# Performance work log

Measured on AMD Instinct MI355X. Metric: run time of the kernel, lower is better.

## Reference

```python
import jax, jax.numpy as jnp
import numpy as np

N = 100000
SEQ = 12
DIMS = [32, 64, 64, 32]


def _glorot(key, shape):
    fan_in, fan_out = shape[0], shape[1]
    lim = jnp.sqrt(6.0 / (fan_in + fan_out))
    return jax.random.uniform(key, shape, jnp.float32, -lim, lim)


def setup_inputs() -> dict:
    key = jax.random.key(0)
    ks = jax.random.split(key, 8)
    x = jax.random.normal(ks[0], (N, DIMS[0], 1), dtype=jnp.float32)
    spiral_indices = jax.random.randint(ks[1], (N, SEQ), 0, N)
    # SpiralConv i: Linear(SEQ * DIMS[i], DIMS[i+1])
    W0 = _glorot(ks[2], (SEQ * DIMS[0], DIMS[1]))
    b0 = jnp.zeros((DIMS[1],), jnp.float32)
    W1 = _glorot(ks[3], (SEQ * DIMS[1], DIMS[2]))
    b1 = jnp.zeros((DIMS[2],), jnp.float32)
    W2 = _glorot(ks[4], (SEQ * DIMS[2], DIMS[3]))
    b2 = jnp.zeros((DIMS[3],), jnp.float32)
    return {"x": x, "spiral_indices": spiral_indices,
            "W0": W0, "b0": b0, "W1": W1, "b1": b1, "W2": W2, "b2": b2}


def _spiral_conv(h, idx, W, b):
    # h: [N, C]; idx: [N, SEQ] -> gathered [N, SEQ, C] -> flat [N, SEQ*C]
    n = h.shape[0]
    g = jnp.take(h, idx, axis=0).reshape(n, -1)
    return g @ W + b


def reference(x, spiral_indices, W0, b0, W1, b1, W2, b2):
    h = x[..., 0]  # squeeze(-1): [N, C_in]
    h = jax.nn.elu(_spiral_conv(h, spiral_indices, W0, b0))
    h = jax.nn.elu(_spiral_conv(h, spiral_indices, W1, b1))
    h = _spiral_conv(h, spiral_indices, W2, b2)  # final_activation=False
    return h[:, :, None]
```

## Files before the change

kernel.cpp:

```cpp
#include <hip/hip_runtime.h>
#include <math.h>


typedef __bf16 bf16;
typedef bf16  bf16x4 __attribute__((ext_vector_type(4)));
typedef bf16  bf16x8 __attribute__((ext_vector_type(8)));
typedef float f32x4  __attribute__((ext_vector_type(4)));

template<int CIN, int COUT>
__device__ inline void pack_one(const float* __restrict__ W, bf16* __restrict__ BP, int e) {
    constexpr int NT = COUT / 16, CC = CIN / 32;
    const int f = e >> 9, r = e & 511, lane = r >> 3, j = r & 7;
    const int t = f % NT, cc = (f / NT) % CC, s = f / (NT * CC);
    const int col = t * 16 + (lane & 15);
    const int k   = s * CIN + cc * 32 + (lane >> 4) * 8 + j;
    BP[e] = (bf16)W[k * COUT + col];
}

__global__ __launch_bounds__(256)
void prep_all(const float* __restrict__ x, bf16* __restrict__ xb,
              const float* __restrict__ W0, const float* __restrict__ W1,
              const float* __restrict__ W2, bf16* __restrict__ B0,
              bf16* __restrict__ B1, bf16* __restrict__ B2, int n)
{
    const int gid = blockIdx.x * 256 + threadIdx.x;
    const int e = gid * 4;
    if (e < n * 32) {
        const f32x4 v = *reinterpret_cast<const f32x4*>(x + e);
        bf16x4 o = {(bf16)v[0], (bf16)v[1], (bf16)v[2], (bf16)v[3]};
        *reinterpret_cast<bf16x4*>(xb + e) = o;
    }
    if (gid < 384 * 64)                       pack_one<32, 64>(W0, B0, gid);
    else if (gid < 384 * 64 + 768 * 64)       pack_one<64, 64>(W1, B1, gid - 384 * 64);
    else if (gid < 384 * 64 + 768 * 64 + 768 * 32)
                                              pack_one<64, 32>(W2, B2, gid - 384 * 64 - 768 * 64);
}

template<int CIN, int COUT, bool ELU, typename TOUT>
__global__ __launch_bounds__(256, 3)
void spiral_mfma(const bf16* __restrict__ h, const int* __restrict__ idx,
                 const bf16* __restrict__ BP, const float* __restrict__ bias,
                 TOUT* __restrict__ out, int n)
{
    constexpr int CC  = CIN / 32;
    constexpr int NT  = COUT / 16;
    constexpr int PS  = CIN * COUT;
    constexpr int SC  = 12 / CC;
    constexpr int NCH = 12 / SC;
    constexpr int PL  = 12;

    __shared__ bf16 Bs[SC * PS];

    const int tid  = threadIdx.x;
    const int lane = tid & 63;
    const int wave = tid >> 6;
    const int m    = lane & 15;
    const int quad = lane >> 4;
    const int i0   = (blockIdx.x * 4 + wave) * 32;
    const bool valid = (i0 < n);

    const int ir0 = min(i0 + m,      n - 1);
    const int ir1 = min(i0 + 16 + m, n - 1);
    const int4* p0 = reinterpret_cast<const int4*>(idx + (size_t)ir0 * 12);
    const int4* p1 = reinterpret_cast<const int4*>(idx + (size_t)ir1 * 12);
    const int4 q00 = p0[0], q01 = p0[1], q02 = p0[2];
    const int4 q10 = p1[0], q11 = p1[1], q12 = p1[2];
    const int rg0[12] = {q00.x,q00.y,q00.z,q00.w, q01.x,q01.y,q01.z,q01.w, q02.x,q02.y,q02.z,q02.w};
    const int rg1[12] = {q10.x,q10.y,q10.z,q10.w, q11.x,q11.y,q11.z,q11.w, q12.x,q12.y,q12.z,q12.w};

    f32x4 acc0[NT] = {}, acc1[NT] = {};

    #pragma unroll
    for (int c = 0; c < NCH; ++c) {
        if (c) __syncthreads();
        const bf16* src = BP + (size_t)c * SC * PS;
        #pragma unroll
        for (int r2 = tid; r2 < SC * PS / 8; r2 += 256)
            *reinterpret_cast<bf16x8*>(&Bs[r2 * 8]) =
                *reinterpret_cast<const bf16x8*>(&src[r2 * 8]);
        __syncthreads();

        {
            bf16x8 a[PL];
            #pragma unroll
            for (int sl = 0; sl < SC; ++sl)
                #pragma unroll
                for (int cc = 0; cc < CC; ++cc)
                    a[sl * CC + cc] = *reinterpret_cast<const bf16x8*>(
                        h + (size_t)rg0[c * SC + sl] * CIN + cc * 32 + quad * 8);
            __builtin_amdgcn_sched_barrier(0);
            #pragma unroll
            for (int p = 0; p < PL; ++p)
                #pragma unroll
                for (int t = 0; t < NT; ++t) {
                    const bf16x8 b = *reinterpret_cast<const bf16x8*>(
                        &Bs[(p * NT + t) * 512 + lane * 8]);
                    acc0[t] = __builtin_amdgcn_mfma_f32_16x16x32_bf16(a[p], b, acc0[t], 0, 0, 0);
                }
        }
        {
            bf16x8 a[PL];
            #pragma unroll
            for (int sl = 0; sl < SC; ++sl)
                #pragma unroll
                for (int cc = 0; cc < CC; ++cc)
                    a[sl * CC + cc] = *reinterpret_cast<const bf16x8*>(
                        h + (size_t)rg1[c * SC + sl] * CIN + cc * 32 + quad * 8);
            __builtin_amdgcn_sched_barrier(0);
            #pragma unroll
            for (int p = 0; p < PL; ++p)
                #pragma unroll
                for (int t = 0; t < NT; ++t) {
                    const bf16x8 b = *reinterpret_cast<const bf16x8*>(
                        &Bs[(p * NT + t) * 512 + lane * 8]);
                    acc1[t] = __builtin_amdgcn_mfma_f32_16x16x32_bf16(a[p], b, acc1[t], 0, 0, 0);
                }
        }
    }

    if (!valid) return;

    #pragma unroll
    for (int t = 0; t < NT; ++t) {
        const int col = t * 16 + m;
        const float bv = bias[col];
        #pragma unroll
        for (int g = 0; g < 4; ++g) {
            {
                const int row = i0 + quad * 4 + g;
                float v = acc0[t][g] + bv;
                if (ELU) v = (v > 0.f) ? v : (__expf(v) - 1.f);
                out[(size_t)row * COUT + col] = (TOUT)v;
            }
            {
                const int row = i0 + 16 + quad * 4 + g;
                float v = acc1[t][g] + bv;
                if (ELU) v = (v > 0.f) ? v : (__expf(v) - 1.f);
                out[(size_t)row * COUT + col] = (TOUT)v;
            }
        }
    }
}

extern "C" void kernel_launch(void* const* d_in, const int* in_sizes, int n_in,
                              void* d_out, int out_size, void* d_ws, size_t ws_size,
                              hipStream_t stream) {
    const float* x   = (const float*)d_in[0];
    const int*   idx = (const int*)d_in[1];
    const float* W0  = (const float*)d_in[2];
    const float* b0  = (const float*)d_in[3];
    const float* W1  = (const float*)d_in[4];
    const float* b1  = (const float*)d_in[5];
    const float* W2  = (const float*)d_in[6];
    const float* b2  = (const float*)d_in[7];
    float* out = (float*)d_out;

    const int n = in_sizes[0] / 32;

    bf16* xb = (bf16*)d_ws;
    bf16* h1 = xb + (size_t)n * 32;
    bf16* h2 = h1 + (size_t)n * 64;
    bf16* B0 = h2 + (size_t)n * 64;
    bf16* B1 = B0 + 384 * 64;
    bf16* B2 = B1 + 768 * 64;

    const int prep_threads = n * 8;
    prep_all<<<(prep_threads + 255) / 256, dim3(256), 0, stream>>>(x, xb, W0, W1, W2, B0, B1, B2, n);

    const int grid = (n + 127) / 128;
    spiral_mfma<32, 64, true,  bf16 ><<<grid, dim3(256), 0, stream>>>(xb, idx, B0, b0, h1,  n);
    spiral_mfma<64, 64, true,  bf16 ><<<grid, dim3(256), 0, stream>>>(h1, idx, B1, b1, h2,  n);
    spiral_mfma<64, 32, false, float><<<grid, dim3(256), 0, stream>>>(h2, idx, B2, b2, out, n);
}
```

Before: 169.4 us.

## Halve rows per wave and shrink weight staging chunk for higher occupancy

Each wave now handles 16 rows instead of 32, so a block covers 64 rows and the grid doubles. The weight slice staged in shared memory per chunk is halved (6 A-fragments per chunk instead of 12), which cuts LDS use and registers so the launch bound can request 5 blocks per CU instead of 3. The aim is more waves in flight to hide the latency of the random row gathers. In exchange, every weight chunk is copied from global memory into LDS twice as often per output row, and there are more barriers per row computed.

Result: faster. 157.8 us (-6.9%).

```diff
diff --git a/kernel.cpp b/kernel.cpp
--- a/kernel.cpp
+++ b/kernel.cpp
@@ -37,7 +37,7 @@
 }
 
 template<int CIN, int COUT, bool ELU, typename TOUT>
-__global__ __launch_bounds__(256, 3)
+__global__ __launch_bounds__(256, 5)
 void spiral_mfma(const bf16* __restrict__ h, const int* __restrict__ idx,
                  const bf16* __restrict__ BP, const float* __restrict__ bias,
                  TOUT* __restrict__ out, int n)
@@ -45,9 +45,9 @@
     constexpr int CC  = CIN / 32;
     constexpr int NT  = COUT / 16;
     constexpr int PS  = CIN * COUT;
-    constexpr int SC  = 12 / CC;
+    constexpr int SC  = 6 / CC;
     constexpr int NCH = 12 / SC;
-    constexpr int PL  = 12;
+    constexpr int PL  = 6;
 
     __shared__ bf16 Bs[SC * PS];
 
@@ -56,19 +56,15 @@
     const int wave = tid >> 6;
     const int m    = lane & 15;
     const int quad = lane >> 4;
-    const int i0   = (blockIdx.x * 4 + wave) * 32;
+    const int i0   = (blockIdx.x * 4 + wave) * 16;
     const bool valid = (i0 < n);
 
-    const int ir0 = min(i0 + m,      n - 1);
-    const int ir1 = min(i0 + 16 + m, n - 1);
-    const int4* p0 = reinterpret_cast<const int4*>(idx + (size_t)ir0 * 12);
-    const int4* p1 = reinterpret_cast<const int4*>(idx + (size_t)ir1 * 12);
-    const int4 q00 = p0[0], q01 = p0[1], q02 = p0[2];
-    const int4 q10 = p1[0], q11 = p1[1], q12 = p1[2];
-    const int rg0[12] = {q00.x,q00.y,q00.z,q00.w, q01.x,q01.y,q01.z,q01.w, q02.x,q02.y,q02.z,q02.w};
-    const int rg1[12] = {q10.x,q10.y,q10.z,q10.w, q11.x,q11.y,q11.z,q11.w, q12.x,q12.y,q12.z,q12.w};
+    const int ir = min(i0 + m, n - 1);
+    const int4* ip = reinterpret_cast<const int4*>(idx + (size_t)ir * 12);
+    const int4 q0 = ip[0], q1 = ip[1], q2 = ip[2];
+    const int rg[12] = {q0.x,q0.y,q0.z,q0.w, q1.x,q1.y,q1.z,q1.w, q2.x,q2.y,q2.z,q2.w};
 
-    f32x4 acc0[NT] = {}, acc1[NT] = {};
+    f32x4 acc[NT] = {};
 
     #pragma unroll
     for (int c = 0; c < NCH; ++c) {
@@ -80,42 +76,22 @@
                 *reinterpret_cast<const bf16x8*>(&src[r2 * 8]);
         __syncthreads();
 
-        {
-            bf16x8 a[PL];
+        bf16x8 a[PL];
+        #pragma unroll
+        for (int sl = 0; sl < SC; ++sl)
             #pragma unroll
-            for (int sl = 0; sl < SC; ++sl)
-                #pragma unroll
-                for (int cc = 0; cc < CC; ++cc)
-                    a[sl * CC + cc] = *reinterpret_cast<const bf16x8*>(
-                        h + (size_t)rg0[c * SC + sl] * CIN + cc * 32 + quad * 8);
-            __builtin_amdgcn_sched_barrier(0);
+            for (int cc = 0; cc < CC; ++cc)
+                a[sl * CC + cc] = *reinterpret_cast<const bf16x8*>(
+                    h + (size_t)rg[c * SC + sl] * CIN + cc * 32 + quad * 8);
+        __builtin_amdgcn_sched_barrier(0);
+        #pragma unroll
+        for (int p = 0; p < PL; ++p)
             #pragma unroll
-            for (int p = 0; p < PL; ++p)
-                #pragma unroll
-                for (int t = 0; t < NT; ++t) {
-                    const bf16x8 b = *reinterpret_cast<const bf16x8*>(
-                        &Bs[(p * NT + t) * 512 + lane * 8]);
-                    acc0[t] = __builtin_amdgcn_mfma_f32_16x16x32_bf16(a[p], b, acc0[t], 0, 0, 0);
-                }
-        }
-        {
-            bf16x8 a[PL];
-            #pragma unroll
-            for (int sl = 0; sl < SC; ++sl)
-                #pragma unroll
-                for (int cc = 0; cc < CC; ++cc)
-                    a[sl * CC + cc] = *reinterpret_cast<const bf16x8*>(
-                        h + (size_t)rg1[c * SC + sl] * CIN + cc * 32 + quad * 8);
-            __builtin_amdgcn_sched_barrier(0);
-            #pragma unroll
-            for (int p = 0; p < PL; ++p)
-                #pragma unroll
-                for (int t = 0; t < NT; ++t) {
-                    const bf16x8 b = *reinterpret_cast<const bf16x8*>(
-                        &Bs[(p * NT + t) * 512 + lane * 8]);
-                    acc1[t] = __builtin_amdgcn_mfma_f32_16x16x32_bf16(a[p], b, acc1[t], 0, 0, 0);
-                }
-        }
+            for (int t = 0; t < NT; ++t) {
+                const bf16x8 b = *reinterpret_cast<const bf16x8*>(
+                    &Bs[(p * NT + t) * 512 + lane * 8]);
+                acc[t] = __builtin_amdgcn_mfma_f32_16x16x32_bf16(a[p], b, acc[t], 0, 0, 0);
+            }
     }
 
     if (!valid) return;
@@ -126,18 +102,10 @@
         const float bv = bias[col];
         #pragma unroll
         for (int g = 0; g < 4; ++g) {
-            {
-                const int row = i0 + quad * 4 + g;
-                float v = acc0[t][g] + bv;
-                if (ELU) v = (v > 0.f) ? v : (__expf(v) - 1.f);
-                out[(size_t)row * COUT + col] = (TOUT)v;
-            }
-            {
-                const int row = i0 + 16 + quad * 4 + g;
-                float v = acc1[t][g] + bv;
-                if (ELU) v = (v > 0.f) ? v : (__expf(v) - 1.f);
-                out[(size_t)row * COUT + col] = (TOUT)v;
-            }
+            const int row = i0 + quad * 4 + g;
+            float v = acc[t][g] + bv;
+            if (ELU) v = (v > 0.f) ? v : (__expf(v) - 1.f);
+            out[(size_t)row * COUT + col] = (TOUT)v;
         }
     }
 }
@@ -167,7 +135,7 @@
     const int prep_threads = n * 8;
     prep_all<<<(prep_threads + 255) / 256, dim3(256), 0, stream>>>(x, xb, W0, W1, W2, B0, B1, B2, n);
 
-    const int grid = (n + 127) / 128;
+    const int grid = (n + 63) / 64;
     spiral_mfma<32, 64, true,  bf16 ><<<grid, dim3(256), 0, stream>>>(xb, idx, B0, b0, h1,  n);
     spiral_mfma<64, 64, true,  bf16 ><<<grid, dim3(256), 0, stream>>>(h1, idx, B1, b1, h2,  n);
     spiral_mfma<64, 32, false, float><<<grid, dim3(256), 0, stream>>>(h2, idx, B2, b2, out, n);
```
